# Performance work log

Measured on AMD Instinct MI355X. Metric: run time of the kernel, lower is better.

Reference implementation:

```python
import jax, jax.numpy as jnp
import numpy as np

NUM_NODES = 200000
NUM_EDGES = 300000
NUM_QUERIES = 128
NUM_ENTITIES = 50000
N_DIMS = 256
N_DIMS_SM = 64
STATIC_DIM = 128
STATIC_SM = 32
G_IN = 2 * N_DIMS_SM + STATIC_SM + N_DIMS_SM  # 224


def leaky(x):
    return jnp.where(x > 0, x, 0.01 * x)


def setup_inputs() -> dict:
    key = jax.random.key(0)
    ks = jax.random.split(key, 24)
    W = 0.05  # weight scale to keep logits in a sane range
    inp = {
        'memorized_embedding': jax.random.normal(ks[0], (NUM_NODES, N_DIMS), jnp.float32),
        'node_score': jax.random.uniform(ks[1], (NUM_NODES,), jnp.float32),
        'rel_emb': jax.random.normal(ks[2], (NUM_EDGES, N_DIMS), jnp.float32),
        'query_src_ts_emb': jax.random.normal(ks[3], (NUM_QUERIES, STATIC_DIM), jnp.float32),
        'query_rel_emb': jax.random.normal(ks[4], (NUM_QUERIES, N_DIMS), jnp.float32),
        'eg_idx': jax.random.randint(ks[5], (NUM_EDGES,), 0, NUM_QUERIES, jnp.int32),
        'src_idx': jax.random.randint(ks[6], (NUM_EDGES,), 0, NUM_NODES, jnp.int32),
        'dst_idx': jax.random.randint(ks[7], (NUM_EDGES,), 0, NUM_NODES, jnp.int32),
        'entity_idx': jax.random.randint(ks[8], (NUM_NODES,), 0, NUM_ENTITIES, jnp.int32),
        'W_proj': W * jax.random.normal(ks[9], (N_DIMS, N_DIMS_SM), jnp.float32),
        'b_proj': W * jax.random.normal(ks[10], (N_DIMS_SM,), jnp.float32),
        'W_static': W * jax.random.normal(ks[11], (STATIC_DIM, STATIC_SM), jnp.float32),
        'b_static': W * jax.random.normal(ks[12], (STATIC_SM,), jnp.float32),
        'W_bs': W * jax.random.normal(ks[13], (N_DIMS, N_DIMS), jnp.float32),
        'b_bs': W * jax.random.normal(ks[14], (N_DIMS,), jnp.float32),
        'Wl': W * jax.random.normal(ks[15], (G_IN, N_DIMS_SM), jnp.float32),
        'bl': W * jax.random.normal(ks[16], (N_DIMS_SM,), jnp.float32),
        'Wr': W * jax.random.normal(ks[17], (G_IN, N_DIMS_SM), jnp.float32),
        'br': W * jax.random.normal(ks[18], (N_DIMS_SM,), jnp.float32),
        'Wc': W * jax.random.normal(ks[19], (N_DIMS_SM, N_DIMS_SM), jnp.float32),
        'bc': W * jax.random.normal(ks[20], (N_DIMS_SM,), jnp.float32),
    }
    return inp


def reference(memorized_embedding, node_score, rel_emb, query_src_ts_emb, query_rel_emb,
              eg_idx, src_idx, dst_idx, entity_idx,
              W_proj, b_proj, W_static, b_static, W_bs, b_bs,
              Wl, bl, Wr, br, Wc, bc):
    # one attention-flow step: linear_between_steps -> attention scoring (G) ->
    # per-source-node softmax -> attention propagation -> per-entity aggregation
    emb2 = leaky(memorized_embedding @ W_bs + b_bs)        # [N, d]
    # project all node embeddings once (linear commutes with gather)
    proj_all = emb2 @ W_proj + b_proj                       # [N, d_sm]
    hvi = proj_all[src_idx]                                 # [E, d_sm]
    hvj = proj_all[dst_idx]                                 # [E, d_sm]
    rel = rel_emb @ W_proj + b_proj                         # [E, d_sm]
    # context_dim_red
    qs = query_src_ts_emb @ W_static + b_static             # [B, static_sm]
    qr = query_rel_emb @ W_proj + b_proj                    # [B, d_sm]
    qs_e = qs[eg_idx]                                       # [E, static_sm]
    qr_e = qr[eg_idx]                                       # [E, d_sm]
    left = jnp.concatenate([hvi, rel, qs_e, qr_e], axis=-1)   # [E, G_IN]
    right = jnp.concatenate([hvj, rel, qs_e, qr_e], axis=-1)  # [E, G_IN]
    # G: sum(leaky(left W_l) * ((leaky(right W_r)) W_c))
    lh = leaky(left @ Wl + bl)                              # [E, d_sm]
    rh = leaky(right @ Wr + br) @ Wc + bc                   # [E, d_sm]
    logits = jnp.sum(lh * rh, axis=-1)                      # [E]
    # transition probability: softmax over outgoing edges of each source node
    seg_max = jax.ops.segment_max(logits, src_idx, num_segments=NUM_NODES)
    ex = jnp.exp(logits - seg_max[src_idx])
    denom = jax.ops.segment_sum(ex, src_idx, num_segments=NUM_NODES)
    trans = ex / denom[src_idx]
    # propagate node attention along edges (node_score_aggregation='sum')
    new_node_score = jax.ops.segment_sum(trans * node_score[src_idx], dst_idx,
                                         num_segments=NUM_NODES)
    # _aggregate_op_entity: sparse COO matmul == segment_sum over entity groups
    entity_att_score = jax.ops.segment_sum(new_node_score, entity_idx,
                                           num_segments=NUM_ENTITIES)
    return entity_att_score
```

## Files before the change

### kernel.cpp

```cpp
#include <hip/hip_runtime.h>
#include <hip/hip_bf16.h>

#define N_NODES 200000
#define N_EDGES 300000
#define N_Q     128
#define N_ENT   50000
#define D       256
#define DSM     64
#define SDIM    128
#define SSM     32

typedef __attribute__((ext_vector_type(8))) short bf16x8;
typedef __attribute__((ext_vector_type(4))) float f32x4;

__device__ __forceinline__ float leaky(float x){ return x > 0.f ? x : 0.01f*x; }

__device__ __forceinline__ unsigned short f2bf(float f){
  __hip_bfloat16 h = __float2bfloat16(f);
  return *reinterpret_cast<unsigned short*>(&h);
}
__device__ __forceinline__ unsigned pk2bf(float a, float b){
  float2 t; t.x = a; t.y = b;
  __hip_bfloat162 h = __float22bfloat162_rn(t);
  return *reinterpret_cast<unsigned*>(&h);
}
__device__ __forceinline__ float bf2f(unsigned short h){
  return __uint_as_float(((unsigned)h) << 16);
}

__device__ __forceinline__ void dev_pack(const float* __restrict__ src,
                                         unsigned short* __restrict__ dst,
                                         int K, int N, int id, int total){
  if (id >= total) return;
  int lane = id & 63, fb = id >> 6;
  int KB = K >> 5;
  int kb = fb % KB, nb = fb / KB;
  int k0 = kb*32 + ((lane>>4)<<3);
  int n  = nb*16 + (lane & 15);
  #pragma unroll
  for (int i = 0; i < 8; ++i) dst[(size_t)id*8 + i] = f2bf(src[(size_t)(k0+i)*N + n]);
}

__global__ void k_setup1(float* out, float* denom,
                         const float* __restrict__ Wp, const float* __restrict__ Wl,
                         const float* __restrict__ Wr, float* Wnlr, float* Wrlr,
                         const float* __restrict__ bp, float* cv,
                         const float* __restrict__ qsrc, const float* __restrict__ Ws,
                         const float* __restrict__ bs, const float* __restrict__ qrel,
                         float* qs, float* qr,
                         const float* __restrict__ Wbs, unsigned short* Wbs_pk,
                         const float* __restrict__ Wc, unsigned short* Wc_pk){
  int b = blockIdx.x, tid = threadIdx.x;
  if (b < 782){
    int id = b*256 + tid;
    if (id < N_ENT) out[id] = 0.f;
    if (id < N_NODES) denom[id] = 0.f;
  } else if (b < 1038){
    int id = (b-782)*256 + tid;
    int m = id >> 14, rem = id & 16383, k = rem >> 6, c = rem & 63;
    const float* Wsrc = (m & 1) ? Wr : Wl;
    int roff = (m >> 1) * 64;
    float s = 0.f;
    for (int i = 0; i < 64; ++i) s += Wp[k*64+i] * Wsrc[(roff+i)*64 + c];
    float* o = (m >> 1) ? Wrlr : Wnlr;
    o[k*128 + (m&1)*64 + c] = s;
  } else if (b == 1038){
    int m = tid >> 6, c = tid & 63;
    const float* Wsrc = (m & 1) ? Wr : Wl;
    int roff = (m >> 1) * 64;
    float s = 0.f;
    for (int i = 0; i < 64; ++i) s += bp[i] * Wsrc[(roff+i)*64 + c];
    cv[tid] = s;
  } else if (b < 1087){
    int id = (b-1039)*256 + tid;
    if (id < N_Q*SSM){
      int q = id >> 5, i = id & 31;
      float s = bs[i];
      for (int j = 0; j < SDIM; ++j) s += qsrc[q*SDIM+j] * Ws[j*SSM+i];
      qs[id] = s;
    } else {
      int id2 = id - N_Q*SSM;
      int q = id2 >> 6, i = id2 & 63;
      float s = bp[i];
      for (int j = 0; j < D; ++j) s += qrel[q*D+j] * Wp[j*DSM+i];
      qr[id2] = s;
    }
  } else if (b < 1119){
    dev_pack(Wbs, Wbs_pk, 256, 256, (b-1087)*256 + tid, 8192);
  } else {
    dev_pack(Wc, Wc_pk, 64, 64, (b-1119)*256 + tid, 512);
  }
}

__global__ void k_setup2(const float* __restrict__ qs, const float* __restrict__ qr,
                         const float* __restrict__ Wl, const float* __restrict__ bl,
                         const float* __restrict__ Wr, const float* __restrict__ br,
                         unsigned* qctx_p,
                         const float* __restrict__ Wnlr, unsigned short* Wn_pk,
                         const float* __restrict__ Wrlr, unsigned short* Wr_pk){
  int b = blockIdx.x, tid = threadIdx.x;
  if (b < 32){
    int id = b*256 + tid;
    int q = id >> 6, c = id & 63;
    float sl = bl[c], sr = br[c];
    for (int i = 0; i < SSM; ++i){
      float v = qs[q*SSM+i];
      sl += v * Wl[(128+i)*64+c];
      sr += v * Wr[(128+i)*64+c];
    }
    for (int i = 0; i < DSM; ++i){
      float v = qr[q*DSM+i];
      sl += v * Wl[(160+i)*64+c];
      sr += v * Wr[(160+i)*64+c];
    }
    qctx_p[id] = pk2bf(sl, sr);
  } else if (b < 48){
    dev_pack(Wnlr, Wn_pk, 256, 128, (b-32)*256 + tid, 4096);
  } else {
    dev_pack(Wrlr, Wr_pk, 256, 128, (b-48)*256 + tid, 4096);
  }
}

__global__ __launch_bounds__(256) void k_node(const float* __restrict__ A,
    const unsigned short* __restrict__ Wbs_pk, const float* __restrict__ bbs,
    const unsigned short* __restrict__ Wn_pk, const float* __restrict__ cv,
    unsigned short* __restrict__ node_l, unsigned short* __restrict__ node_r){
  __shared__ char smem[32768];
  int tid = threadIdx.x;
  int row0 = blockIdx.x * 64;
  {
    const float4* Ag = (const float4*)(A + (size_t)row0 * 256);
    #pragma unroll
    for (int it = 0; it < 16; ++it){
      int f = tid + 256*it;
      int r = f >> 6, c4 = f & 63;
      float4 v = Ag[f];
      uint2 u;
      u.x = pk2bf(v.x, v.y);
      u.y = pk2bf(v.z, v.w);
      int byte = (r << 9) + (c4 << 3);
      byte ^= (r & 7) << 4;
      *(uint2*)(smem + byte) = u;
    }
  }
  __syncthreads();
  int l = tid & 63, wn = tid >> 6;
  f32x4 acc[4][4];
  #pragma unroll
  for (int mf = 0; mf < 4; ++mf)
    #pragma unroll
    for (int nf = 0; nf < 4; ++nf) acc[mf][nf] = (f32x4){0.f,0.f,0.f,0.f};
  for (int kb = 0; kb < 8; ++kb){
    bf16x8 a[4], b[4];
    #pragma unroll
    for (int mf = 0; mf < 4; ++mf){
      int row = mf*16 + (l & 15);
      int byte = (row << 9) + kb*64 + ((l >> 4) << 4);
      byte ^= (row & 7) << 4;
      a[mf] = *(const bf16x8*)(smem + byte);
    }
    #pragma unroll
    for (int nf = 0; nf < 4; ++nf){
      int nb = wn*4 + nf;
      b[nf] = *(const bf16x8*)(Wbs_pk + ((size_t)(nb*8 + kb)*64 + l)*8);
    }
    #pragma unroll
    for (int mf = 0; mf < 4; ++mf)
      #pragma unroll
      for (int nf = 0; nf < 4; ++nf)
        acc[mf][nf] = __builtin_amdgcn_mfma_f32_16x16x32_bf16(a[mf], b[nf], acc[mf][nf], 0, 0, 0);
  }
  __syncthreads();
  #pragma unroll
  for (int mf = 0; mf < 4; ++mf)
    #pragma unroll
    for (int nf = 0; nf < 4; ++nf){
      int col = wn*64 + nf*16 + (l & 15);
      float bb = bbs[col];
      #pragma unroll
      for (int r = 0; r < 4; ++r){
        int row = mf*16 + ((l >> 4) << 2) + r;
        int byte = (row << 9) + col*2;
        byte ^= (row & 7) << 4;
        *(unsigned short*)(smem + byte) = f2bf(leaky(acc[mf][nf][r] + bb));
      }
    }
  __syncthreads();
  f32x4 acc2[4][2];
  #pragma unroll
  for (int mf = 0; mf < 4; ++mf){ acc2[mf][0] = (f32x4){0.f,0.f,0.f,0.f}; acc2[mf][1] = (f32x4){0.f,0.f,0.f,0.f}; }
  for (int kb = 0; kb < 8; ++kb){
    bf16x8 a[4], b[2];
    #pragma unroll
    for (int mf = 0; mf < 4; ++mf){
      int row = mf*16 + (l & 15);
      int byte = (row << 9) + kb*64 + ((l >> 4) << 4);
      byte ^= (row & 7) << 4;
      a[mf] = *(const bf16x8*)(smem + byte);
    }
    #pragma unroll
    for (int nf = 0; nf < 2; ++nf){
      int nb = wn*2 + nf;
      b[nf] = *(const bf16x8*)(Wn_pk + ((size_t)(nb*8 + kb)*64 + l)*8);
    }
    #pragma unroll
    for (int mf = 0; mf < 4; ++mf)
      #pragma unroll
      for (int nf = 0; nf < 2; ++nf)
        acc2[mf][nf] = __builtin_amdgcn_mfma_f32_16x16x32_bf16(a[mf], b[nf], acc2[mf][nf], 0, 0, 0);
  }
  #pragma unroll
  for (int mf = 0; mf < 4; ++mf)
    #pragma unroll
    for (int nf = 0; nf < 2; ++nf){
      int col = wn*32 + nf*16 + (l & 15);
      float cc = cv[col];
      #pragma unroll
      for (int r = 0; r < 4; ++r){
        int row = mf*16 + ((l >> 4) << 2) + r;
        unsigned short h = f2bf(acc2[mf][nf][r] + cc);
        size_t g = (size_t)(row0 + row);
        if (col < 64) node_l[g*64 + col] = h;
        else          node_r[g*64 + col - 64] = h;
      }
    }
}

__global__ __launch_bounds__(256) void k_edge(const float* __restrict__ relE,
    const unsigned short* __restrict__ Wr_pk, const unsigned short* __restrict__ Wc_pk,
    const float* __restrict__ cv, const float* __restrict__ bc,
    const unsigned short* __restrict__ node_l, const unsigned short* __restrict__ node_r,
    const unsigned* __restrict__ qctx_p,
    const int* __restrict__ src, const int* __restrict__ dst, const int* __restrict__ eg,
    float* __restrict__ exbuf, float* __restrict__ denom){
  __shared__ char smem[32768];
  int tid = threadIdx.x;
  int l = tid & 63, wn = tid >> 6;
  char* wbase = smem + wn*8192;
  char* sRL  = wbase;
  char* sLc  = wbase + 4096;
  char* sRin = wbase + 6144;
  int e0 = blockIdx.x * 64 + wn*16;

  int idxv;
  {
    int j = l & 15;
    int e = e0 + j;
    int ec = e < N_EDGES ? e : N_EDGES-1;
    const int* p = (l < 16) ? src : (l < 32) ? dst : eg;
    idxv = p[ec];
  }
  int arow = e0 + (l & 15);
  if (arow >= N_EDGES) arow = N_EDGES - 1;
  const float4* Rg = (const float4*)relE;
  size_t rbase = (size_t)arow * 64 + ((l >> 4) << 1);
  float4 av0[8], av1[8];
  #pragma unroll
  for (int kb = 0; kb < 8; ++kb){
    av0[kb] = Rg[rbase + kb*8];
    av1[kb] = Rg[rbase + kb*8 + 1];
  }
  unsigned short nlv[16], nrv[16];
  unsigned qpv[16];
  #pragma unroll
  for (int j = 0; j < 16; ++j){
    int s  = __shfl(idxv, j);
    int d2 = __shfl(idxv, 16 + j);
    int b  = __shfl(idxv, 32 + j);
    nlv[j] = node_l[(size_t)s*64 + l];
    nrv[j] = node_r[(size_t)d2*64 + l];
    qpv[j] = qctx_p[b*64 + l];
  }

  f32x4 acc[8];
  #pragma unroll
  for (int nb = 0; nb < 8; ++nb) acc[nb] = (f32x4){0.f,0.f,0.f,0.f};
  #pragma unroll
  for (int kb = 0; kb < 8; ++kb){
    union { bf16x8 v; unsigned u[4]; } au;
    au.u[0] = pk2bf(av0[kb].x, av0[kb].y); au.u[1] = pk2bf(av0[kb].z, av0[kb].w);
    au.u[2] = pk2bf(av1[kb].x, av1[kb].y); au.u[3] = pk2bf(av1[kb].z, av1[kb].w);
    #pragma unroll
    for (int nb = 0; nb < 8; ++nb){
      bf16x8 b = *(const bf16x8*)(Wr_pk + ((size_t)(nb*8 + kb)*64 + l)*8);
      acc[nb] = __builtin_amdgcn_mfma_f32_16x16x32_bf16(au.v, b, acc[nb], 0, 0, 0);
    }
  }
  #pragma unroll
  for (int nb = 0; nb < 8; ++nb){
    int col = nb*16 + (l & 15);
    float cc = cv[128 + col];
    #pragma unroll
    for (int r = 0; r < 4; ++r){
      int row = ((l >> 4) << 2) + r;
      int byte = (row << 8) + (col << 1);
      byte ^= (row & 12) << 3;
      *(unsigned short*)(sRL + byte) = f2bf(acc[nb][r] + cc);
    }
  }
  #pragma unroll
  for (int j = 0; j < 16; ++j){
    int e = e0 + j;
    int byteL = (j << 8) + (l << 1);        byteL ^= (j & 12) << 3;
    int byteR = (j << 8) + ((64+l) << 1);   byteR ^= (j & 12) << 3;
    int bL = (j << 7) + (l << 1);           bL ^= (j & 12) << 3;
    int bR = (j << 7) + (l << 1);           bR ^= (j & 7) << 4;
    unsigned short lh16 = 0, rr16 = 0;
    if (e < N_EDGES){
      unsigned qv = qpv[j];
      float lh = leaky(bf2f(nlv[j]) + bf2f(*(unsigned short*)(sRL + byteL))
                       + bf2f((unsigned short)(qv & 0xFFFFu)));
      float rr = leaky(bf2f(nrv[j]) + bf2f(*(unsigned short*)(sRL + byteR))
                       + bf2f((unsigned short)(qv >> 16)));
      lh16 = f2bf(lh); rr16 = f2bf(rr);
    }
    *(unsigned short*)(sLc + bL) = lh16;
    *(unsigned short*)(sRin + bR) = rr16;
  }
  float bcv[4];
  #pragma unroll
  for (int nf = 0; nf < 4; ++nf) bcv[nf] = bc[nf*16 + (l & 15)];
  f32x4 acc2[4];
  #pragma unroll
  for (int nf = 0; nf < 4; ++nf) acc2[nf] = (f32x4){0.f,0.f,0.f,0.f};
  #pragma unroll
  for (int kb = 0; kb < 2; ++kb){
    int row = l & 15;
    int byte = (row << 7) + kb*64 + ((l >> 4) << 4);
    byte ^= (row & 7) << 4;
    bf16x8 a = *(const bf16x8*)(sRin + byte);
    #pragma unroll
    for (int nf = 0; nf < 4; ++nf){
      bf16x8 bfr = *(const bf16x8*)(Wc_pk + ((size_t)(nf*2 + kb)*64 + l)*8);
      acc2[nf] = __builtin_amdgcn_mfma_f32_16x16x32_bf16(a, bfr, acc2[nf], 0, 0, 0);
    }
  }
  int srcj[4];
  float vr[4];
  #pragma unroll
  for (int r = 0; r < 4; ++r){
    int rowl = ((l >> 4) << 2) + r;
    srcj[r] = __shfl(idxv, rowl);
    float v = 0.f;
    #pragma unroll
    for (int nf = 0; nf < 4; ++nf){
      int col = nf*16 + (l & 15);
      int byte = (rowl << 7) + (col << 1);
      byte ^= (rowl & 12) << 3;
      v += (acc2[nf][r] + bcv[nf]) * bf2f(*(unsigned short*)(sLc + byte));
    }
    v += __shfl_xor(v, 1); v += __shfl_xor(v, 2);
    v += __shfl_xor(v, 4); v += __shfl_xor(v, 8);
    vr[r] = v;
  }
  if ((l & 15) == 0){
    #pragma unroll
    for (int r = 0; r < 4; ++r){
      int rowl = ((l >> 4) << 2) + r;
      int e = e0 + rowl;
      if (e < N_EDGES){
        float ex = __expf(vr[r]);
        exbuf[e] = ex;
        atomicAdd(&denom[srcj[r]], ex);
      }
    }
  }
}

__global__ void k_passC(const float* __restrict__ exbuf, const float* __restrict__ denom,
                        const int* __restrict__ src, const int* __restrict__ dst,
                        const float* __restrict__ node_score, const int* __restrict__ ent,
                        float* __restrict__ out){
  int e = blockIdx.x*256 + threadIdx.x;
  if (e >= N_EDGES) return;
  int s = src[e];
  float tr = exbuf[e] / denom[s];
  atomicAdd(&out[ent[dst[e]]], tr * node_score[s]);
}

extern "C" void kernel_launch(void* const* d_in, const int* in_sizes, int n_in,
                              void* d_out, int out_size, void* d_ws, size_t ws_size,
                              hipStream_t stream){
  const float* mem   = (const float*)d_in[0];
  const float* nsc   = (const float*)d_in[1];
  const float* relE  = (const float*)d_in[2];
  const float* qsrc  = (const float*)d_in[3];
  const float* qrel  = (const float*)d_in[4];
  const int*   eg    = (const int*)d_in[5];
  const int*   src   = (const int*)d_in[6];
  const int*   dst   = (const int*)d_in[7];
  const int*   ent   = (const int*)d_in[8];
  const float* Wp    = (const float*)d_in[9];
  const float* bp    = (const float*)d_in[10];
  const float* Ws    = (const float*)d_in[11];
  const float* bs    = (const float*)d_in[12];
  const float* Wbs   = (const float*)d_in[13];
  const float* bbs   = (const float*)d_in[14];
  const float* Wl    = (const float*)d_in[15];
  const float* bl    = (const float*)d_in[16];
  const float* Wr    = (const float*)d_in[17];
  const float* br    = (const float*)d_in[18];
  const float* Wc    = (const float*)d_in[19];
  const float* bc    = (const float*)d_in[20];
  float* out = (float*)d_out;

  char* w = (char*)d_ws;
  auto alloc = [&](size_t bytes)->void*{
    void* p = (void*)w; w += (bytes + 255) & ~(size_t)255; return p;
  };
  float* Wnlr = (float*)alloc(32768*4);
  float* Wrlr = (float*)alloc(32768*4);
  unsigned short* Wbs_pk = (unsigned short*)alloc(65536*2);
  unsigned short* Wn_pk  = (unsigned short*)alloc(32768*2);
  unsigned short* Wr_pk  = (unsigned short*)alloc(32768*2);
  unsigned short* Wc_pk  = (unsigned short*)alloc(4096*2);
  float* cv  = (float*)alloc(256*4);
  float* qs  = (float*)alloc((size_t)N_Q*SSM*4);
  float* qr  = (float*)alloc((size_t)N_Q*DSM*4);
  unsigned* qctx_p = (unsigned*)alloc((size_t)N_Q*DSM*4);
  unsigned short* node_l = (unsigned short*)alloc((size_t)N_NODES*64*2);
  unsigned short* node_r = (unsigned short*)alloc((size_t)N_NODES*64*2);
  float* exbuf  = (float*)alloc((size_t)N_EDGES*4);
  float* denom = (float*)alloc((size_t)N_NODES*4);

  k_setup1<<<1121, 256, 0, stream>>>(out, denom,
                                     Wp, Wl, Wr, Wnlr, Wrlr, bp, cv,
                                     qsrc, Ws, bs, qrel, qs, qr,
                                     Wbs, Wbs_pk, Wc, Wc_pk);
  k_setup2<<<64, 256, 0, stream>>>(qs, qr, Wl, bl, Wr, br, qctx_p,
                                   Wnlr, Wn_pk, Wrlr, Wr_pk);
  k_node<<<N_NODES/64, 256, 0, stream>>>(mem, Wbs_pk, bbs, Wn_pk, cv, node_l, node_r);
  k_edge<<<(N_EDGES+63)/64, 256, 0, stream>>>(relE, Wr_pk, Wc_pk, cv, bc,
                                              node_l, node_r, qctx_p,
                                              src, dst, eg, exbuf, denom);
  k_passC<<<(N_EDGES+255)/256, 256, 0, stream>>>(exbuf, denom, src, dst, nsc, ent, out);
}
```

Before: 263.7 us.

## Stage rel_emb rows through LDS with double-buffered loads to cut register pressure

The edge kernel used to hold each wave's full 16x256 fp32 rel_emb tile in 64 registers per lane before converting to bf16 for MFMA. It now loads rows in coalesced chunks of four, double-buffered, converts them to bf16 and writes them into a swizzled LDS region. The A fragments are then read back from LDS. The query-context gather moves to the point of use, and launch bounds ask for three blocks per SM, so fewer registers are live and occupancy can rise. The cost is extra LDS traffic, a serial chunk loop, and a wait on LDS before the epilogue.

After: 293.3 us. 11.2% more time.

```diff
diff --git a/kernel.cpp b/kernel.cpp
--- a/kernel.cpp
+++ b/kernel.cpp
@@ -226,7 +226,7 @@
     }
 }
 
-__global__ __launch_bounds__(256) void k_edge(const float* __restrict__ relE,
+__global__ __launch_bounds__(256, 3) void k_edge(const float* __restrict__ relE,
     const unsigned short* __restrict__ Wr_pk, const unsigned short* __restrict__ Wc_pk,
     const float* __restrict__ cv, const float* __restrict__ bc,
     const unsigned short* __restrict__ node_l, const unsigned short* __restrict__ node_r,
@@ -250,42 +250,61 @@
     const int* p = (l < 16) ? src : (l < 32) ? dst : eg;
     idxv = p[ec];
   }
-  int arow = e0 + (l & 15);
-  if (arow >= N_EDGES) arow = N_EDGES - 1;
-  const float4* Rg = (const float4*)relE;
-  size_t rbase = (size_t)arow * 64 + ((l >> 4) << 1);
-  float4 av0[8], av1[8];
-  #pragma unroll
-  for (int kb = 0; kb < 8; ++kb){
-    av0[kb] = Rg[rbase + kb*8];
-    av1[kb] = Rg[rbase + kb*8 + 1];
-  }
   unsigned short nlv[16], nrv[16];
-  unsigned qpv[16];
   #pragma unroll
   for (int j = 0; j < 16; ++j){
     int s  = __shfl(idxv, j);
     int d2 = __shfl(idxv, 16 + j);
-    int b  = __shfl(idxv, 32 + j);
     nlv[j] = node_l[(size_t)s*64 + l];
     nrv[j] = node_r[(size_t)d2*64 + l];
-    qpv[j] = qctx_p[b*64 + l];
-  }
-
+  }
+  {
+    const float4* Rg = (const float4*)relE;
+    float4 va[4], vb[4];
+    #pragma unroll
+    for (int i = 0; i < 4; ++i){
+      int ge = e0 + i; if (ge >= N_EDGES) ge = N_EDGES-1;
+      va[i] = Rg[(size_t)ge*64 + l];
+    }
+    #pragma unroll 1
+    for (int c = 0; c < 4; ++c){
+      if (c < 3){
+        #pragma unroll
+        for (int i = 0; i < 4; ++i){
+          int ge = e0 + (c+1)*4 + i; if (ge >= N_EDGES) ge = N_EDGES-1;
+          vb[i] = Rg[(size_t)ge*64 + l];
+        }
+      }
+      #pragma unroll
+      for (int i = 0; i < 4; ++i){
+        int r = c*4 + i;
+        uint2 u;
+        u.x = pk2bf(va[i].x, va[i].y);
+        u.y = pk2bf(va[i].z, va[i].w);
+        int byte = (r << 9) + (l << 3);
+        byte ^= (r & 7) << 4;
+        *(uint2*)(wbase + byte) = u;
+        va[i] = vb[i];
+      }
+    }
+  }
   f32x4 acc[8];
   #pragma unroll
   for (int nb = 0; nb < 8; ++nb) acc[nb] = (f32x4){0.f,0.f,0.f,0.f};
   #pragma unroll
   for (int kb = 0; kb < 8; ++kb){
-    union { bf16x8 v; unsigned u[4]; } au;
-    au.u[0] = pk2bf(av0[kb].x, av0[kb].y); au.u[1] = pk2bf(av0[kb].z, av0[kb].w);
-    au.u[2] = pk2bf(av1[kb].x, av1[kb].y); au.u[3] = pk2bf(av1[kb].z, av1[kb].w);
+    int row = l & 15;
+    int byte = (row << 9) + kb*64 + ((l >> 4) << 4);
+    byte ^= (row & 7) << 4;
+    bf16x8 a = *(const bf16x8*)(wbase + byte);
     #pragma unroll
     for (int nb = 0; nb < 8; ++nb){
       bf16x8 b = *(const bf16x8*)(Wr_pk + ((size_t)(nb*8 + kb)*64 + l)*8);
-      acc[nb] = __builtin_amdgcn_mfma_f32_16x16x32_bf16(au.v, b, acc[nb], 0, 0, 0);
-    }
-  }
+      acc[nb] = __builtin_amdgcn_mfma_f32_16x16x32_bf16(a, b, acc[nb], 0, 0, 0);
+    }
+  }
+  asm volatile("s_waitcnt lgkmcnt(0)" ::: "memory");
+  __builtin_amdgcn_sched_barrier(0);
   #pragma unroll
   for (int nb = 0; nb < 8; ++nb){
     int col = nb*16 + (l & 15);
@@ -307,7 +326,8 @@
     int bR = (j << 7) + (l << 1);           bR ^= (j & 7) << 4;
     unsigned short lh16 = 0, rr16 = 0;
     if (e < N_EDGES){
-      unsigned qv = qpv[j];
+      int b = __shfl(idxv, 32 + j);
+      unsigned qv = qctx_p[b*64 + l];
       float lh = leaky(bf2f(nlv[j]) + bf2f(*(unsigned short*)(sRL + byteL))
                        + bf2f((unsigned short)(qv & 0xFFFFu)));
       float rr = leaky(bf2f(nrv[j]) + bf2f(*(unsigned short*)(sRL + byteR))
```
